# Kernel optimization log

Hardware: AMD Instinct MI355X
Metric: run time of the kernel (lower is better)

Reference implementation:

```python
import jax, jax.numpy as jnp
import numpy as np

B, S, D = 32, 2048, 1024
H = 8
D_ATTN = 256
D_HEAD = D_ATTN // H          # 32
D_HEAD_OUT = D // H           # 128
SOFTMAX_TEMP = 1.0


def setup_inputs() -> dict:
    key = jax.random.key(0)
    k0, k1, k2, k3, k4 = jax.random.split(key, 5)
    features = jax.random.normal(k0, (B, S, D), dtype=jnp.float32)
    # truncated-normal(std=0.01) init approximated with scaled normal
    w1 = jax.random.normal(k1, (H, D, D_HEAD), dtype=jnp.float32) * 0.01
    b1 = jax.random.normal(k2, (H, D_HEAD), dtype=jnp.float32) * 0.01
    w2 = jax.random.normal(k3, (H, D_HEAD, D_HEAD_OUT), dtype=jnp.float32) * 0.01
    b2 = jax.random.normal(k4, (H, D_HEAD_OUT), dtype=jnp.float32) * 0.01
    return {"features": features, "w1": w1, "b1": b1, "w2": w2, "b2": b2}


def reference(features, w1, b1, w2, b2):
    Bc, Sc, Dc = features.shape
    # per-head first projection: [B,H,S,d_head]
    h = jnp.einsum('bsd,hde->bhse', features, w1) + b1[None, :, None, :]
    h = jax.nn.gelu(h, approximate=False)  # torch nn.GELU default is exact erf
    # second projection: [B,H,S,d_head_out]
    logits = jnp.einsum('bhse,heo->bhso', h, w2) + b2[None, :, None, :]
    # softmax over seq dim (axis=2)
    smw = jax.nn.softmax(logits / SOFTMAX_TEMP, axis=2)
    # [B,H,S,D/H] -> [B,S,H,D/H] -> [B,S,D]
    smw = smw.transpose(0, 2, 1, 3).reshape(Bc, Sc, Dc)
    return (features * smw).sum(axis=1)  # [B,D]
```

## Files before the change

kernel.cpp:

```cpp
#include <hip/hip_runtime.h>
#include <math.h>

#define S_  2048
#define D_  1024

typedef __attribute__((ext_vector_type(8))) short short8;
typedef __attribute__((ext_vector_type(4))) float f32x4;

static __device__ __forceinline__ unsigned short f2bf(float x) {
    unsigned int u = __builtin_bit_cast(unsigned int, x);
    u += 0x7fffu + ((u >> 16) & 1u);
    return (unsigned short)(u >> 16);
}
static __device__ __forceinline__ float bf2f(unsigned short s) {
    unsigned int u = ((unsigned int)s) << 16;
    return __builtin_bit_cast(float, u);
}

__device__ __forceinline__ void gl_lds16(const void* g, void* l) {
    __builtin_amdgcn_global_load_lds(
        (const __attribute__((address_space(1))) unsigned int*)g,
        (__attribute__((address_space(3))) unsigned int*)l, 16, 0, 0);
}

__global__ void prep_w1(const float* __restrict__ w1, short* __restrict__ w1p) {
    int tid = blockIdx.x * 256 + threadIdx.x;
    int lane = tid & 63;
    int fragid = tid >> 6;
    int cf = fragid & 15, ks = fragid >> 4;
    int col = cf * 16 + (lane & 15);
    int h = col >> 5, e = col & 31;
    int d0 = ks * 32 + (lane >> 4) * 8;
    short8 v;
#pragma unroll
    for (int r = 0; r < 8; ++r)
        v[r] = (short)f2bf(w1[((size_t)h * D_ + (d0 + r)) * 32 + e]);
    *(short8*)(w1p + (size_t)tid * 8) = v;
}

__global__ void prep_w2(const float* __restrict__ w2, short* __restrict__ w2p) {
    int tid = blockIdx.x * 256 + threadIdx.x;
    int lane = tid & 63;
    int fragid = tid >> 6;
    int cf2 = fragid & 7, h = fragid >> 3;
    int o = cf2 * 16 + (lane & 15);
    int e0 = (lane >> 4) * 8;
    short8 v;
#pragma unroll
    for (int r = 0; r < 8; ++r)
        v[r] = (short)f2bf(w2[((size_t)h * 32 + (e0 + r)) * 128 + o]);
    *(short8*)(w2p + (size_t)tid * 8) = v;
}

__global__ __launch_bounds__(256) void fused1(
        const float* __restrict__ feat,
        const short* __restrict__ w1p,
        const short* __restrict__ w2p,
        const float* __restrict__ b1,
        const float* __restrict__ b2,
        unsigned short* __restrict__ E)
{
    __shared__ __align__(16) char lds[66816];
    short* Bbuf = (short*)lds;
    short* hact = (short*)(lds + 33024);
    unsigned short* Est = (unsigned short*)lds;

    const int tid = threadIdx.x;
    const int wv = tid >> 6;
    const int lane = tid & 63;
    const int lr = lane & 15;
    const int lg = lane >> 4;
    const size_t m0 = (size_t)blockIdx.x * 64;

    const f32x4* Arow = (const f32x4*)(feat + (m0 + (size_t)(wv * 16 + lr)) * D_);

    const f32x4 vzero = {0.f, 0.f, 0.f, 0.f};
    f32x4 acc[16];
#pragma unroll
    for (int i = 0; i < 16; ++i) acc[i] = vzero;

    auto stageB = [&](int buf_, int ks_) {
#pragma unroll
        for (int j = 0; j < 4; ++j)
            gl_lds16(w1p + (size_t)ks_ * 8192 + (size_t)(j * 256 + tid) * 8,
                     Bbuf + buf_ * 8192 + (j * 256 + wv * 64) * 8);
    };

    stageB(0, 0);
    int buf = 0;
    for (int ks = 0; ks < 32; ++ks) {
        __syncthreads();
        if (ks + 1 < 32) stageB(buf ^ 1, ks + 1);

        f32x4 a0 = Arow[ks * 8 + lg * 2 + 0];
        f32x4 a1 = Arow[ks * 8 + lg * 2 + 1];
        short8 af;
        af[0] = (short)f2bf(a0.x); af[1] = (short)f2bf(a0.y);
        af[2] = (short)f2bf(a0.z); af[3] = (short)f2bf(a0.w);
        af[4] = (short)f2bf(a1.x); af[5] = (short)f2bf(a1.y);
        af[6] = (short)f2bf(a1.z); af[7] = (short)f2bf(a1.w);

        const short8* Bf = (const short8*)(Bbuf + buf * 8192);
#pragma unroll
        for (int cf = 0; cf < 16; ++cf) {
            short8 bfr = Bf[cf * 64 + lane];
            acc[cf] = __builtin_amdgcn_mfma_f32_16x16x32_bf16(af, bfr, acc[cf], 0, 0, 0);
        }
        buf ^= 1;
    }

#pragma unroll
    for (int cf = 0; cf < 16; ++cf) {
        const int col = cf * 16 + lr;
        const float bias = b1[col];
#pragma unroll
        for (int r = 0; r < 4; ++r) {
            const int row = wv * 16 + lg * 4 + r;
            float x = acc[cf][r] + bias;
            float g = 0.5f * x * (1.0f + erff(x * 0.70710678118654752f));
            hact[row * 264 + col] = (short)f2bf(g);
        }
    }

    short8 bw[16];
    float bias2[16];
#pragma unroll
    for (int cf = 0; cf < 16; ++cf) {
        const int h = 2 * wv + (cf >> 3);
        const int cf2 = cf & 7;
        bw[cf] = *(const short8*)(w2p + ((size_t)(h * 8 + cf2) * 64 + lane) * 8);
        bias2[cf] = b2[h * 128 + cf2 * 16 + lr];
    }
    __syncthreads();

    for (int rf = 0; rf < 4; ++rf) {
        short8 ah0 = *(const short8*)(hact + (rf * 16 + lr) * 264 + (2 * wv + 0) * 32 + lg * 8);
        short8 ah1 = *(const short8*)(hact + (rf * 16 + lr) * 264 + (2 * wv + 1) * 32 + lg * 8);
#pragma unroll
        for (int cf = 0; cf < 16; ++cf) {
            f32x4 c = vzero;
            c = __builtin_amdgcn_mfma_f32_16x16x32_bf16((cf < 8) ? ah0 : ah1, bw[cf], c, 0, 0, 0);
            const int colL = wv * 256 + (cf >> 3) * 128 + (cf & 7) * 16 + lr;
#pragma unroll
            for (int r = 0; r < 4; ++r) {
                float e = __expf(c[r] + bias2[cf]);
                Est[(lg * 4 + r) * 1032 + colL] = f2bf(e);
            }
        }
        __syncthreads();
#pragma unroll
        for (int j = 0; j < 8; ++j) {
            const int idx = j * 256 + tid;
            const int row = idx >> 7;
            const int ch = idx & 127;
            short8 v = *(const short8*)(Est + row * 1032 + ch * 8);
            *(short8*)(E + (m0 + (size_t)(rf * 16 + row)) * 1024 + ch * 8) = v;
        }
        __syncthreads();
    }
}

__global__ __launch_bounds__(256) void finalize(
        const float* __restrict__ feat,
        const unsigned short* __restrict__ E,
        float* __restrict__ out)
{
    const int b = blockIdx.x >> 4;
    const int chunk = blockIdx.x & 15;
    const int t = threadIdx.x;
    const int cl = t & 63;
    const int q = t >> 6;

    const float* fp = feat + ((size_t)b * S_ + (size_t)q * 512) * D_ + chunk * 64 + cl;
    const unsigned short* ep = E + ((size_t)b * S_ + (size_t)q * 512) * 1024 + chunk * 64 + cl;

    float num = 0.f, den = 0.f;
#pragma unroll 8
    for (int i = 0; i < 512; ++i) {
        float f = fp[(size_t)i * D_];
        float e = bf2f(ep[(size_t)i * 1024]);
        num = fmaf(f, e, num);
        den += e;
    }

    __shared__ float sn[256], sd[256];
    sn[t] = num; sd[t] = den;
    __syncthreads();
    if (t < 64) {
        float N  = sn[t] + sn[t + 64] + sn[t + 128] + sn[t + 192];
        float Dn = sd[t] + sd[t + 64] + sd[t + 128] + sd[t + 192];
        out[(size_t)b * D_ + chunk * 64 + t] = N / Dn;
    }
}

extern "C" void kernel_launch(void* const* d_in, const int* in_sizes, int n_in,
                              void* d_out, int out_size, void* d_ws, size_t ws_size,
                              hipStream_t stream) {
    (void)in_sizes; (void)n_in; (void)out_size; (void)ws_size;
    const float* feat = (const float*)d_in[0];
    const float* w1   = (const float*)d_in[1];
    const float* b1   = (const float*)d_in[2];
    const float* w2   = (const float*)d_in[3];
    const float* b2   = (const float*)d_in[4];
    float* out = (float*)d_out;

    char* ws = (char*)d_ws;
    unsigned short* E = (unsigned short*)ws;
    short* w1p = (short*)(ws + 134217728ull);
    short* w2p = (short*)(ws + 134217728ull + 524288ull);

    prep_w1<<<128, 256, 0, stream>>>(w1, w1p);
    prep_w2<<<16, 256, 0, stream>>>(w2, w2p);
    fused1<<<1024, 256, 0, stream>>>(feat, w1p, w2p, b1, b2, E);
    finalize<<<512, 256, 0, stream>>>(feat, E, out);
}
```

Measured before the change: 204.2 us.

## Fuse softmax-weighted reduction into projection kernel, drop E intermediate

The fused kernel now computes exp(logits), multiplies by features, and accumulates per-block numerator and denominator partials directly, instead of writing a bf16 E matrix and re-reading features in a separate finalize pass. A small finalize2 kernel sums the 32 per-block partials per batch. It also retiles the first GEMM into a 2x2 warp layout with register prefetch of A, halves LDS, and adds a launch bound of 4 blocks per CU to raise occupancy. The cost is extra global feature reads inside the epilogue, which should mostly hit cache, and w2 fragments are reloaded per iteration instead of held in registers.

```diff
diff --git a/kernel.cpp b/kernel.cpp
--- a/kernel.cpp
+++ b/kernel.cpp
@@ -11,10 +11,6 @@
     unsigned int u = __builtin_bit_cast(unsigned int, x);
     u += 0x7fffu + ((u >> 16) & 1u);
     return (unsigned short)(u >> 16);
-}
-static __device__ __forceinline__ float bf2f(unsigned short s) {
-    unsigned int u = ((unsigned int)s) << 16;
-    return __builtin_bit_cast(float, u);
 }
 
 __device__ __forceinline__ void gl_lds16(const void* g, void* l) {
@@ -52,32 +48,36 @@
     *(short8*)(w2p + (size_t)tid * 8) = v;
 }
 
-__global__ __launch_bounds__(256) void fused1(
+__global__ __launch_bounds__(256, 4) void fused1(
         const float* __restrict__ feat,
         const short* __restrict__ w1p,
         const short* __restrict__ w2p,
         const float* __restrict__ b1,
         const float* __restrict__ b2,
-        unsigned short* __restrict__ E)
+        float* __restrict__ pnum,
+        float* __restrict__ pden)
 {
-    __shared__ __align__(16) char lds[66816];
+    __shared__ __align__(16) char lds[34816];
     short* Bbuf = (short*)lds;
-    short* hact = (short*)(lds + 33024);
-    unsigned short* Est = (unsigned short*)lds;
+    short* hact = (short*)lds;
 
     const int tid = threadIdx.x;
     const int wv = tid >> 6;
     const int lane = tid & 63;
     const int lr = lane & 15;
     const int lg = lane >> 4;
+    const int wr = wv >> 1, wc = wv & 1;
     const size_t m0 = (size_t)blockIdx.x * 64;
 
-    const f32x4* Arow = (const f32x4*)(feat + (m0 + (size_t)(wv * 16 + lr)) * D_);
+    const f32x4* Arow0 = (const f32x4*)(feat + (m0 + (size_t)(wr * 32 + lr)) * D_);
+    const f32x4* Arow1 = (const f32x4*)(feat + (m0 + (size_t)(wr * 32 + 16 + lr)) * D_);
 
     const f32x4 vzero = {0.f, 0.f, 0.f, 0.f};
-    f32x4 acc[16];
-#pragma unroll
-    for (int i = 0; i < 16; ++i) acc[i] = vzero;
+    f32x4 acc[2][8];
+#pragma unroll
+    for (int i = 0; i < 2; ++i)
+#pragma unroll
+        for (int j = 0; j < 8; ++j) acc[i][j] = vzero;
 
     auto stageB = [&](int buf_, int ks_) {
 #pragma unroll
@@ -87,110 +87,118 @@
     };
 
     stageB(0, 0);
+    f32x4 p00 = Arow0[lg * 2], p01 = Arow0[lg * 2 + 1];
+    f32x4 p10 = Arow1[lg * 2], p11 = Arow1[lg * 2 + 1];
     int buf = 0;
     for (int ks = 0; ks < 32; ++ks) {
         __syncthreads();
         if (ks + 1 < 32) stageB(buf ^ 1, ks + 1);
-
-        f32x4 a0 = Arow[ks * 8 + lg * 2 + 0];
-        f32x4 a1 = Arow[ks * 8 + lg * 2 + 1];
-        short8 af;
-        af[0] = (short)f2bf(a0.x); af[1] = (short)f2bf(a0.y);
-        af[2] = (short)f2bf(a0.z); af[3] = (short)f2bf(a0.w);
-        af[4] = (short)f2bf(a1.x); af[5] = (short)f2bf(a1.y);
-        af[6] = (short)f2bf(a1.z); af[7] = (short)f2bf(a1.w);
+        f32x4 a00 = p00, a01 = p01, a10 = p10, a11 = p11;
+        if (ks + 1 < 32) {
+            const int o = (ks + 1) * 8 + lg * 2;
+            p00 = Arow0[o]; p01 = Arow0[o + 1];
+            p10 = Arow1[o]; p11 = Arow1[o + 1];
+        }
+        short8 af0, af1;
+        af0[0] = (short)f2bf(a00.x); af0[1] = (short)f2bf(a00.y);
+        af0[2] = (short)f2bf(a00.z); af0[3] = (short)f2bf(a00.w);
+        af0[4] = (short)f2bf(a01.x); af0[5] = (short)f2bf(a01.y);
+        af0[6] = (short)f2bf(a01.z); af0[7] = (short)f2bf(a01.w);
+        af1[0] = (short)f2bf(a10.x); af1[1] = (short)f2bf(a10.y);
+        af1[2] = (short)f2bf(a10.z); af1[3] = (short)f2bf(a10.w);
+        af1[4] = (short)f2bf(a11.x); af1[5] = (short)f2bf(a11.y);
+        af1[6] = (short)f2bf(a11.z); af1[7] = (short)f2bf(a11.w);
 
         const short8* Bf = (const short8*)(Bbuf + buf * 8192);
 #pragma unroll
-        for (int cf = 0; cf < 16; ++cf) {
-            short8 bfr = Bf[cf * 64 + lane];
-            acc[cf] = __builtin_amdgcn_mfma_f32_16x16x32_bf16(af, bfr, acc[cf], 0, 0, 0);
+        for (int cf = 0; cf < 8; ++cf) {
+            short8 bfr = Bf[(wc * 8 + cf) * 64 + lane];
+            acc[0][cf] = __builtin_amdgcn_mfma_f32_16x16x32_bf16(af0, bfr, acc[0][cf], 0, 0, 0);
+            acc[1][cf] = __builtin_amdgcn_mfma_f32_16x16x32_bf16(af1, bfr, acc[1][cf], 0, 0, 0);
         }
         buf ^= 1;
     }
 
-#pragma unroll
-    for (int cf = 0; cf < 16; ++cf) {
-        const int col = cf * 16 + lr;
+    __syncthreads();
+
+#pragma unroll
+    for (int rf1 = 0; rf1 < 2; ++rf1)
+#pragma unroll
+    for (int cf = 0; cf < 8; ++cf) {
+        const int col = wc * 128 + cf * 16 + lr;
         const float bias = b1[col];
 #pragma unroll
         for (int r = 0; r < 4; ++r) {
-            const int row = wv * 16 + lg * 4 + r;
-            float x = acc[cf][r] + bias;
+            const int row = wr * 32 + rf1 * 16 + lg * 4 + r;
+            float x = acc[rf1][cf][r] + bias;
             float g = 0.5f * x * (1.0f + erff(x * 0.70710678118654752f));
             hact[row * 264 + col] = (short)f2bf(g);
         }
     }
-
-    short8 bw[16];
+    __syncthreads();
+
     float bias2[16];
 #pragma unroll
     for (int cf = 0; cf < 16; ++cf) {
         const int h = 2 * wv + (cf >> 3);
-        const int cf2 = cf & 7;
-        bw[cf] = *(const short8*)(w2p + ((size_t)(h * 8 + cf2) * 64 + lane) * 8);
-        bias2[cf] = b2[h * 128 + cf2 * 16 + lr];
-    }
-    __syncthreads();
+        bias2[cf] = b2[h * 128 + (cf & 7) * 16 + lr];
+    }
+    float num_acc[16], den_acc[16];
+#pragma unroll
+    for (int cf = 0; cf < 16; ++cf) { num_acc[cf] = 0.f; den_acc[cf] = 0.f; }
 
     for (int rf = 0; rf < 4; ++rf) {
         short8 ah0 = *(const short8*)(hact + (rf * 16 + lr) * 264 + (2 * wv + 0) * 32 + lg * 8);
         short8 ah1 = *(const short8*)(hact + (rf * 16 + lr) * 264 + (2 * wv + 1) * 32 + lg * 8);
 #pragma unroll
         for (int cf = 0; cf < 16; ++cf) {
+            const int h = 2 * wv + (cf >> 3);
+            short8 bw = *(const short8*)(w2p + ((size_t)(h * 8 + (cf & 7)) * 64 + lane) * 8);
             f32x4 c = vzero;
-            c = __builtin_amdgcn_mfma_f32_16x16x32_bf16((cf < 8) ? ah0 : ah1, bw[cf], c, 0, 0, 0);
-            const int colL = wv * 256 + (cf >> 3) * 128 + (cf & 7) * 16 + lr;
+            c = __builtin_amdgcn_mfma_f32_16x16x32_bf16((cf < 8) ? ah0 : ah1, bw, c, 0, 0, 0);
+            const int col = wv * 256 + (cf >> 3) * 128 + (cf & 7) * 16 + lr;
 #pragma unroll
             for (int r = 0; r < 4; ++r) {
-                float e = __expf(c[r] + bias2[cf]);
-                Est[(lg * 4 + r) * 1032 + colL] = f2bf(e);
+                const float e = __expf(c[r] + bias2[cf]);
+                const int row = rf * 16 + lg * 4 + r;
+                const float f = feat[(m0 + row) * D_ + col];
+                den_acc[cf] += e;
+                num_acc[cf] = fmaf(f, e, num_acc[cf]);
             }
         }
-        __syncthreads();
-#pragma unroll
-        for (int j = 0; j < 8; ++j) {
-            const int idx = j * 256 + tid;
-            const int row = idx >> 7;
-            const int ch = idx & 127;
-            short8 v = *(const short8*)(Est + row * 1032 + ch * 8);
-            *(short8*)(E + (m0 + (size_t)(rf * 16 + row)) * 1024 + ch * 8) = v;
-        }
-        __syncthreads();
-    }
-}
-
-__global__ __launch_bounds__(256) void finalize(
-        const float* __restrict__ feat,
-        const unsigned short* __restrict__ E,
+    }
+
+    const size_t pb = (size_t)blockIdx.x * 1024;
+#pragma unroll
+    for (int cf = 0; cf < 16; ++cf) {
+        float dn = den_acc[cf];
+        dn += __shfl_xor(dn, 16); dn += __shfl_xor(dn, 32);
+        float nm = num_acc[cf];
+        nm += __shfl_xor(nm, 16); nm += __shfl_xor(nm, 32);
+        if (lg == 0) {
+            const int col = wv * 256 + (cf >> 3) * 128 + (cf & 7) * 16 + lr;
+            pden[pb + col] = dn;
+            pnum[pb + col] = nm;
+        }
+    }
+}
+
+__global__ __launch_bounds__(256) void finalize2(
+        const float* __restrict__ pnum,
+        const float* __restrict__ pden,
         float* __restrict__ out)
 {
-    const int b = blockIdx.x >> 4;
-    const int chunk = blockIdx.x & 15;
-    const int t = threadIdx.x;
-    const int cl = t & 63;
-    const int q = t >> 6;
-
-    const float* fp = feat + ((size_t)b * S_ + (size_t)q * 512) * D_ + chunk * 64 + cl;
-    const unsigned short* ep = E + ((size_t)b * S_ + (size_t)q * 512) * 1024 + chunk * 64 + cl;
-
-    float num = 0.f, den = 0.f;
+    const int idx = blockIdx.x * 256 + threadIdx.x;
+    const int b = idx >> 10;
+    const int d = idx & 1023;
+    const size_t base = (size_t)b * 32 * 1024 + d;
+    float n = 0.f, dn = 0.f;
 #pragma unroll 8
-    for (int i = 0; i < 512; ++i) {
-        float f = fp[(size_t)i * D_];
-        float e = bf2f(ep[(size_t)i * 1024]);
-        num = fmaf(f, e, num);
-        den += e;
-    }
-
-    __shared__ float sn[256], sd[256];
-    sn[t] = num; sd[t] = den;
-    __syncthreads();
-    if (t < 64) {
-        float N  = sn[t] + sn[t + 64] + sn[t + 128] + sn[t + 192];
-        float Dn = sd[t] + sd[t + 64] + sd[t + 128] + sd[t + 192];
-        out[(size_t)b * D_ + chunk * 64 + t] = N / Dn;
-    }
+    for (int j = 0; j < 32; ++j) {
+        n  += pnum[base + (size_t)j * 1024];
+        dn += pden[base + (size_t)j * 1024];
+    }
+    out[idx] = n / dn;
 }
 
 extern "C" void kernel_launch(void* const* d_in, const int* in_sizes, int n_in,
@@ -205,12 +213,13 @@
     float* out = (float*)d_out;
 
     char* ws = (char*)d_ws;
-    unsigned short* E = (unsigned short*)ws;
-    short* w1p = (short*)(ws + 134217728ull);
-    short* w2p = (short*)(ws + 134217728ull + 524288ull);
+    float* pnum = (float*)ws;
+    float* pden = (float*)(ws + (4ull << 20));
+    short* w1p  = (short*)(ws + (8ull << 20));
+    short* w2p  = (short*)(ws + (8ull << 20) + (512ull << 10));
 
     prep_w1<<<128, 256, 0, stream>>>(w1, w1p);
     prep_w2<<<16, 256, 0, stream>>>(w2, w2p);
-    fused1<<<1024, 256, 0, stream>>>(feat, w1p, w2p, b1, b2, E);
-    finalize<<<512, 256, 0, stream>>>(feat, E, out);
-}
+    fused1<<<1024, 256, 0, stream>>>(feat, w1p, w2p, b1, b2, pnum, pden);
+    finalize2<<<128, 256, 0, stream>>>(pnum, pden, out);
+}
```

Result: faster. 174.2 us (-14.7%).
